# Optimization experiments

Measured on AMD Instinct MI355X. Metric: run time of the kernel, lower is better.

## Reference

```python
import jax, jax.numpy as jnp
import numpy as np

N = 50000
E = 800000
F_IN = 512
H = 128
K = 10
ALPHA = 0.1
EPS = 1e-5  # BatchNorm eps


def setup_inputs() -> dict:
    key = jax.random.key(0)
    ks = jax.random.split(key, 16)
    x = jax.random.normal(ks[0], (N, F_IN), dtype=jnp.float32)
    edge_index = jax.random.randint(ks[1], (2, E), 0, N, dtype=jnp.int64)
    # Linear weights (xavier-ish scale)
    W1 = jax.random.normal(ks[2], (F_IN, H), dtype=jnp.float32) * (1.0 / np.sqrt(F_IN))
    b1 = jnp.zeros((H,), dtype=jnp.float32)
    W2 = jax.random.normal(ks[3], (H, H), dtype=jnp.float32) * (1.0 / np.sqrt(H))
    b2 = jnp.zeros((H,), dtype=jnp.float32)
    # BatchNorm (eval mode: running stats)
    gamma1 = jnp.ones((H,), dtype=jnp.float32)
    beta1 = jnp.zeros((H,), dtype=jnp.float32)
    mean1 = jax.random.normal(ks[4], (H,), dtype=jnp.float32) * 0.1
    var1 = jax.random.uniform(ks[5], (H,), dtype=jnp.float32) + 0.5
    gamma2 = jnp.ones((H,), dtype=jnp.float32)
    beta2 = jnp.zeros((H,), dtype=jnp.float32)
    mean2 = jax.random.normal(ks[6], (H,), dtype=jnp.float32) * 0.1
    var2 = jax.random.uniform(ks[7], (H,), dtype=jnp.float32) + 0.5
    return {
        "x": x, "edge_index": edge_index,
        "W1": W1, "b1": b1, "gamma1": gamma1, "beta1": beta1, "mean1": mean1, "var1": var1,
        "W2": W2, "b2": b2, "gamma2": gamma2, "beta2": beta2, "mean2": mean2, "var2": var2,
    }


def _bn_eval(h, gamma, beta, mean, var):
    return (h - mean) * jax.lax.rsqrt(var + EPS) * gamma + beta


def _appnp_prop(h, edge_index):
    # add self loops
    loop = jnp.arange(N, dtype=edge_index.dtype)
    src = jnp.concatenate([edge_index[0], loop])
    dst = jnp.concatenate([edge_index[1], loop])
    # symmetric GCN normalization: deg^{-1/2}[src] * deg^{-1/2}[dst]
    deg = jax.ops.segment_sum(jnp.ones_like(src, dtype=h.dtype), dst, num_segments=N)
    dinv = jax.lax.rsqrt(jnp.maximum(deg, 1.0))
    norm = dinv[src] * dinv[dst]  # [E+N]
    h0 = h

    def step(carry, _):
        msg = carry[src] * norm[:, None]                    # [E+N, H]
        agg = jax.ops.segment_sum(msg, dst, num_segments=N)  # [N, H]
        return (1.0 - ALPHA) * agg + ALPHA * h0, None

    out, _ = jax.lax.scan(step, h, None, length=K)
    return out


def reference(x, edge_index, W1, b1, gamma1, beta1, mean1, var1,
              W2, b2, gamma2, beta2, mean2, var2):
    h = jax.nn.relu(x @ W1 + b1)
    h = _bn_eval(h, gamma1, beta1, mean1, var1)
    # dropout inactive (eval mode)
    h = h @ W2 + b2
    h = _bn_eval(h, gamma2, beta2, mean2, var2)
    return _appnp_prop(h, edge_index)
```

## Files before the change

kernel.cpp:

```cpp
#include <hip/hip_runtime.h>

#define ALPHA_F 0.1f
#define EPS_F   1e-5f

typedef float    f32x4 __attribute__((ext_vector_type(4)));
typedef _Float16 h16x8 __attribute__((ext_vector_type(8)));

__device__ __forceinline__ void gll16(const void* g, void* l)
{
    __builtin_amdgcn_global_load_lds(
        (const __attribute__((address_space(1))) void*)g,
        (__attribute__((address_space(3))) void*)l, 16, 0, 0);
}

__device__ __forceinline__ int pad_cnt(int d) { return (d + 8) & ~7; }

__global__ void convert_wstg(const float* __restrict__ W,
                             _Float16* __restrict__ Wstg, int K)
{
    int idx = blockIdx.x * 256 + threadIdx.x;
    if (idx < K * 128) {
        int k = idx >> 7, n = idx & 127;
        int i = k >> 5, kg = (k >> 3) & 3, j = k & 7;
        Wstg[(size_t)i * 4096 + (kg * 128 + n) * 8 + j] = (_Float16)W[idx];
    }
}

template<bool A_HALF, bool OUT_HALF>
__global__ __launch_bounds__(256) void gemm_stage_bn(
    const void* __restrict__ Av,
    const _Float16* __restrict__ Wstg,
    const float* __restrict__ bias,
    const float* __restrict__ gamma, const float* __restrict__ beta,
    const float* __restrict__ mean,  const float* __restrict__ var,
    void* __restrict__ outv, int M, int K, int do_relu)
{
    __shared__ __align__(16) char Abuf[2][8192];
    __shared__ __align__(16) char Wbuf[2][8192];

    const int t   = threadIdx.x;
    const int w   = t >> 6;
    const int l   = t & 63;
    const int l15 = l & 15;
    const int lk  = l >> 4;
    const int bm  = blockIdx.x * 64;
    const int nk  = K >> 5;
    const int row = w * 16 + l15;

    f32x4 acc[8];
#pragma unroll
    for (int f = 0; f < 8; ++f) acc[f] = (f32x4){0.f, 0.f, 0.f, 0.f};

    auto stage = [&](int buf, int i) {
        const char* wsrc = (const char*)Wstg + (size_t)i * 8192;
#pragma unroll
        for (int c = 0; c < 2; ++c) {
            const int base = w * 128 + c * 64;
            gll16(wsrc + (size_t)(base + l) * 16, &Wbuf[buf][base * 16]);
        }
        if (A_HALF) {
            const int base = w * 64;
            const int sl   = base + l;
            const int r    = sl >> 2;
            const int ch   = (sl & 3) ^ (r & 3);
            int gr = bm + r; gr = (gr < M) ? gr : (M - 1);
            const char* src = (const char*)Av + ((size_t)gr * K + i * 32) * 2
                              + (size_t)ch * 16;
            gll16(src, &Abuf[buf][base * 16]);
        } else {
#pragma unroll
            for (int c = 0; c < 2; ++c) {
                const int base = w * 128 + c * 64;
                const int sl   = base + l;
                const int r    = sl >> 3;
                const int ch   = (sl & 7) ^ (r & 7);
                int gr = bm + r; gr = (gr < M) ? gr : (M - 1);
                const char* src = (const char*)Av + ((size_t)gr * K + i * 32) * 4
                                  + (size_t)ch * 16;
                gll16(src, &Abuf[buf][base * 16]);
            }
        }
    };

    auto compute = [&](int buf) {
        h16x8 a;
        if (A_HALF) {
            a = *(const h16x8*)&Abuf[buf][(row * 4 + (lk ^ (row & 3))) * 16];
        } else {
            f32x4 a0 = *(const f32x4*)&Abuf[buf][(row * 8 + ((2 * lk)     ^ (row & 7))) * 16];
            f32x4 a1 = *(const f32x4*)&Abuf[buf][(row * 8 + ((2 * lk + 1) ^ (row & 7))) * 16];
#pragma unroll
            for (int j = 0; j < 4; ++j) {
                a[j]     = (_Float16)a0[j];
                a[4 + j] = (_Float16)a1[j];
            }
        }
#pragma unroll
        for (int f = 0; f < 8; ++f) {
            h16x8 b = *(const h16x8*)&Wbuf[buf][(lk * 128 + f * 16 + l15) * 16];
            acc[f] = __builtin_amdgcn_mfma_f32_16x16x32_f16(a, b, acc[f], 0, 0, 0);
        }
    };

    stage(0, 0);
    for (int i = 0; i < nk; ++i) {
        __syncthreads();
        if (i + 1 < nk) stage((i + 1) & 1, i + 1);
        compute(i & 1);
    }

#pragma unroll
    for (int f = 0; f < 8; ++f) {
        const int col = f * 16 + l15;
        float s  = gamma[col] * rsqrtf(var[col] + EPS_F);
        float sh = beta[col] - mean[col] * s;
        float bb = bias[col];
#pragma unroll
        for (int rr = 0; rr < 4; ++rr) {
            int rg = bm + w * 16 + lk * 4 + rr;
            if (rg < M) {
                float v = acc[f][rr] + bb;
                if (do_relu) v = fmaxf(v, 0.f);
                v = v * s + sh;
                if (OUT_HALF) ((_Float16*)outv)[(size_t)rg * 128 + col] = (_Float16)v;
                else          ((float*)outv)[(size_t)rg * 128 + col]    = v;
            }
        }
    }
}

__global__ void count_deg(const int* __restrict__ dst, int E, int* __restrict__ deg)
{
    int e = blockIdx.x * 256 + threadIdx.x;
    if (e < E) atomicAdd(&deg[dst[e]], 1);
}

__global__ __launch_bounds__(256) void scan_block_sums(
    const int* __restrict__ deg, int* __restrict__ bsum, int N)
{
    __shared__ int sh[256];
    const int t  = threadIdx.x;
    const int i0 = blockIdx.x * 1024 + t * 4;
    int s = 0;
    if (i0 + 3 < N) {
        int4 d4 = *(const int4*)(deg + i0);
        s = pad_cnt(d4.x) + pad_cnt(d4.y) + pad_cnt(d4.z) + pad_cnt(d4.w);
    } else {
#pragma unroll
        for (int j = 0; j < 4; ++j)
            if (i0 + j < N) s += pad_cnt(deg[i0 + j]);
    }
    sh[t] = s;
    __syncthreads();
#pragma unroll
    for (int d = 128; d > 0; d >>= 1) {
        if (t < d) sh[t] += sh[t + d];
        __syncthreads();
    }
    if (t == 0) bsum[blockIdx.x] = sh[0];
}

__global__ __launch_bounds__(256) void scan_offsets(
    const int* __restrict__ deg, const int* __restrict__ bsum,
    int* __restrict__ offs, int* __restrict__ cursor,
    float* __restrict__ dinv, int N, int B)
{
    __shared__ int sh[256];
    __shared__ int sbase;
    const int b = blockIdx.x, t = threadIdx.x;

    int v = (t < b && t < B) ? bsum[t] : 0;
    sh[t] = v;
    __syncthreads();
#pragma unroll
    for (int d = 128; d > 0; d >>= 1) {
        if (t < d) sh[t] += sh[t + d];
        __syncthreads();
    }
    if (t == 0) sbase = sh[0];
    __syncthreads();

    const int i0 = b * 1024 + t * 4;
    int c[4], s = 0;
#pragma unroll
    for (int j = 0; j < 4; ++j) {
        int i = i0 + j;
        c[j] = (i < N) ? pad_cnt(deg[i]) : 0;
        s += c[j];
    }
    sh[t] = s;
    __syncthreads();
    for (int d = 1; d < 256; d <<= 1) {
        int o = (t >= d) ? sh[t - d] : 0;
        __syncthreads();
        sh[t] += o;
        __syncthreads();
    }
    int run = sbase + sh[t] - s;
#pragma unroll
    for (int j = 0; j < 4; ++j) {
        int i = i0 + j;
        if (i < N) {
            offs[i]   = run;
            cursor[i] = run;
            dinv[i]   = rsqrtf((float)(deg[i] + 1));
            run += c[j];
        }
    }
    if (b == B - 1 && t == 255) offs[N] = run;
}

__global__ void scatter_csr(const int* __restrict__ src, const int* __restrict__ dst,
                            int E, const float* __restrict__ dinv,
                            int* __restrict__ cursor, int2* __restrict__ csr)
{
    int e = blockIdx.x * 256 + threadIdx.x;
    if (e < E) {
        int s = src[e], d = dst[e];
        int pos = atomicAdd(&cursor[d], 1);
        csr[pos] = make_int2(s, __float_as_int(dinv[s] * dinv[d]));
    }
}

__global__ void fill_self_pad(const int* __restrict__ offs, const int* __restrict__ deg,
                              const float* __restrict__ dinv,
                              int2* __restrict__ csr, int N)
{
    int i = blockIdx.x * 256 + threadIdx.x;
    if (i < N) {
        int base = offs[i], d = deg[i], end = offs[i + 1];
        float di = dinv[i];
        csr[base + d] = make_int2(i, __float_as_int(di * di));
        for (int p = base + d + 1; p < end; ++p)
            csr[p] = make_int2(i, 0);
    }
}

__global__ __launch_bounds__(256) void appnp_step(
    const _Float16* __restrict__ cur, const _Float16* __restrict__ h0,
    const int* __restrict__ offs, const int2* __restrict__ csr,
    _Float16* __restrict__ nxt, float* __restrict__ fout, int N)
{
    int wv = (int)((blockIdx.x * 256u + threadIdx.x) >> 6);
    if (wv >= N) return;
    const int i    = __builtin_amdgcn_readfirstlane(wv);
    const int lane = (int)(threadIdx.x & 63u);
    const int g    = lane >> 4;
    const int fl   = (lane & 15) * 8;

    int e   = offs[i];
    int end = offs[i + 1];

    f32x4 accL = (f32x4){0.f, 0.f, 0.f, 0.f};
    f32x4 accH = (f32x4){0.f, 0.f, 0.f, 0.f};

    int4 m = *(const int4*)(csr + e + 2 * g);
    int   iA = m.x,                     iB = m.z;
    float wA = __int_as_float(m.y),     wB = __int_as_float(m.w);
    h16x8 vA = *(const h16x8*)(cur + (size_t)iA * 128 + fl);
    h16x8 vB = *(const h16x8*)(cur + (size_t)iB * 128 + fl);

    for (e += 8; e < end; e += 8) {
        int4 m2 = *(const int4*)(csr + e + 2 * g);
        int   iA2 = m2.x,                 iB2 = m2.z;
        float wA2 = __int_as_float(m2.y), wB2 = __int_as_float(m2.w);
        h16x8 vA2 = *(const h16x8*)(cur + (size_t)iA2 * 128 + fl);
        h16x8 vB2 = *(const h16x8*)(cur + (size_t)iB2 * 128 + fl);
#pragma unroll
        for (int j = 0; j < 4; ++j) {
            accL[j] = fmaf(wA, (float)vA[j],     accL[j]);
            accH[j] = fmaf(wA, (float)vA[4 + j], accH[j]);
            accL[j] = fmaf(wB, (float)vB[j],     accL[j]);
            accH[j] = fmaf(wB, (float)vB[4 + j], accH[j]);
        }
        wA = wA2; wB = wB2; vA = vA2; vB = vB2;
    }
#pragma unroll
    for (int j = 0; j < 4; ++j) {
        accL[j] = fmaf(wA, (float)vA[j],     accL[j]);
        accH[j] = fmaf(wA, (float)vA[4 + j], accH[j]);
        accL[j] = fmaf(wB, (float)vB[j],     accL[j]);
        accH[j] = fmaf(wB, (float)vB[4 + j], accH[j]);
    }

#pragma unroll
    for (int j = 0; j < 4; ++j) {
        accL[j] += __shfl_xor(accL[j], 16);
        accL[j] += __shfl_xor(accL[j], 32);
        accH[j] += __shfl_xor(accH[j], 16);
        accH[j] += __shfl_xor(accH[j], 32);
    }

    if (lane < 16) {
        h16x8 hv = *(const h16x8*)(h0 + (size_t)i * 128 + fl);
        float o[8];
#pragma unroll
        for (int j = 0; j < 4; ++j) {
            o[j]     = ALPHA_F * (float)hv[j]     + (1.f - ALPHA_F) * accL[j];
            o[4 + j] = ALPHA_F * (float)hv[4 + j] + (1.f - ALPHA_F) * accH[j];
        }
        if (fout) {
            f32x4 o0, o1;
#pragma unroll
            for (int j = 0; j < 4; ++j) { o0[j] = o[j]; o1[j] = o[4 + j]; }
            *(f32x4*)(fout + (size_t)i * 128 + fl)     = o0;
            *(f32x4*)(fout + (size_t)i * 128 + fl + 4) = o1;
        } else {
            h16x8 o16;
#pragma unroll
            for (int j = 0; j < 8; ++j) o16[j] = (_Float16)o[j];
            *(h16x8*)(nxt + (size_t)i * 128 + fl) = o16;
        }
    }
}

static inline size_t align_up(size_t x) { return (x + 255) & ~(size_t)255; }

extern "C" void kernel_launch(void* const* d_in, const int* in_sizes, int n_in,
                              void* d_out, int out_size, void* d_ws, size_t ws_size,
                              hipStream_t stream)
{
    const float* x   = (const float*)d_in[0];
    const int*   ei  = (const int*)d_in[1];
    const float* W1  = (const float*)d_in[2];
    const float* b1  = (const float*)d_in[3];
    const float* g1  = (const float*)d_in[4];
    const float* be1 = (const float*)d_in[5];
    const float* m1  = (const float*)d_in[6];
    const float* v1  = (const float*)d_in[7];
    const float* W2  = (const float*)d_in[8];
    const float* b2  = (const float*)d_in[9];
    const float* g2  = (const float*)d_in[10];
    const float* be2 = (const float*)d_in[11];
    const float* m2  = (const float*)d_in[12];
    const float* v2  = (const float*)d_in[13];

    const int N = in_sizes[0] / 512;
    const int E = in_sizes[1] / 2;
    const int* src = ei;
    const int* dst = ei + E;
    const int CSR_CAP = E + 8 * N;
    const int NB = (N + 1023) / 1024;

    char* ws = (char*)d_ws;
    size_t off = 0;
    _Float16* hAh = (_Float16*)(ws + off); off += align_up((size_t)N * 128 * 2);
    _Float16* h0h = (_Float16*)(ws + off); off += align_up((size_t)N * 128 * 2);
    _Float16* p0  = (_Float16*)(ws + off); off += align_up((size_t)N * 128 * 2);
    _Float16* p1  = (_Float16*)(ws + off); off += align_up((size_t)N * 128 * 2);
    int*    deg  = (int*)(ws + off);    off += align_up((size_t)N * 4);
    float*  dinv = (float*)(ws + off);  off += align_up((size_t)N * 4);
    int*    offs = (int*)(ws + off);    off += align_up((size_t)(N + 1) * 4);
    int*    curs = (int*)(ws + off);    off += align_up((size_t)N * 4);
    int*    bsum = (int*)(ws + off);    off += align_up((size_t)256 * 4);
    int2*   csr  = (int2*)(ws + off);   off += align_up((size_t)CSR_CAP * 8);
    _Float16* w1s = (_Float16*)(ws + off); off += align_up((size_t)512 * 128 * 2);
    _Float16* w2s = (_Float16*)(ws + off); off += align_up((size_t)128 * 128 * 2);

    hipMemsetAsync(deg, 0, (size_t)N * 4, stream);
    count_deg<<<(E + 255) / 256, 256, 0, stream>>>(dst, E, deg);
    scan_block_sums<<<NB, 256, 0, stream>>>(deg, bsum, N);
    scan_offsets<<<NB, 256, 0, stream>>>(deg, bsum, offs, curs, dinv, N, NB);
    scatter_csr<<<(E + 255) / 256, 256, 0, stream>>>(src, dst, E, dinv, curs, csr);
    fill_self_pad<<<(N + 255) / 256, 256, 0, stream>>>(offs, deg, dinv, csr, N);

    convert_wstg<<<(512 * 128 + 255) / 256, 256, 0, stream>>>(W1, w1s, 512);
    convert_wstg<<<(128 * 128 + 255) / 256, 256, 0, stream>>>(W2, w2s, 128);

    gemm_stage_bn<false, true><<<(N + 63) / 64, 256, 0, stream>>>(
        x, w1s, b1, g1, be1, m1, v1, hAh, N, 512, 1);
    gemm_stage_bn<true, true><<<(N + 63) / 64, 256, 0, stream>>>(
        hAh, w2s, b2, g2, be2, m2, v2, h0h, N, 128, 0);

    const _Float16* cur = h0h;
    for (int k = 0; k < 10; ++k) {
        _Float16* nxt = (k & 1) ? p1 : p0;
        float* fo = (k == 9) ? (float*)d_out : nullptr;
        appnp_step<<<(N + 3) / 4, 256, 0, stream>>>(
            cur, h0h, offs, csr, nxt, fo, N);
        cur = nxt;
    }

    (void)n_in; (void)out_size; (void)ws_size;
}
```

Baseline: 438.2 us.

## Accumulate APPNP messages in packed fp16 and use persistent grid-stride waves

The propagation step now accumulates neighbor messages with packed half-precision FMAs instead of converting each value to fp32, halving the ALU work in the gather loop. It also launches a fixed grid of 8192 waves that loop over nodes instead of one wave per node, reducing block scheduling overhead. FP16 accumulation over many neighbors across ten iterations risks precision loss, and the fixed grid may reduce latency hiding for this memory-bound gather.

```diff
diff --git a/kernel.cpp b/kernel.cpp
--- a/kernel.cpp
+++ b/kernel.cpp
@@ -5,6 +5,7 @@
 
 typedef float    f32x4 __attribute__((ext_vector_type(4)));
 typedef _Float16 h16x8 __attribute__((ext_vector_type(8)));
+typedef _Float16 h16x2 __attribute__((ext_vector_type(2)));
 
 __device__ __forceinline__ void gll16(const void* g, void* l)
 {
@@ -236,80 +237,89 @@
     }
 }
 
+#define NWAVES 8192
+
 __global__ __launch_bounds__(256) void appnp_step(
     const _Float16* __restrict__ cur, const _Float16* __restrict__ h0,
     const int* __restrict__ offs, const int2* __restrict__ csr,
     _Float16* __restrict__ nxt, float* __restrict__ fout, int N)
 {
-    int wv = (int)((blockIdx.x * 256u + threadIdx.x) >> 6);
-    if (wv >= N) return;
-    const int i    = __builtin_amdgcn_readfirstlane(wv);
+    const int wv0  = __builtin_amdgcn_readfirstlane(
+                        (int)((blockIdx.x * 256u + threadIdx.x) >> 6));
     const int lane = (int)(threadIdx.x & 63u);
     const int g    = lane >> 4;
     const int fl   = (lane & 15) * 8;
 
-    int e   = offs[i];
-    int end = offs[i + 1];
-
-    f32x4 accL = (f32x4){0.f, 0.f, 0.f, 0.f};
-    f32x4 accH = (f32x4){0.f, 0.f, 0.f, 0.f};
-
-    int4 m = *(const int4*)(csr + e + 2 * g);
-    int   iA = m.x,                     iB = m.z;
-    float wA = __int_as_float(m.y),     wB = __int_as_float(m.w);
-    h16x8 vA = *(const h16x8*)(cur + (size_t)iA * 128 + fl);
-    h16x8 vB = *(const h16x8*)(cur + (size_t)iB * 128 + fl);
-
-    for (e += 8; e < end; e += 8) {
-        int4 m2 = *(const int4*)(csr + e + 2 * g);
-        int   iA2 = m2.x,                 iB2 = m2.z;
-        float wA2 = __int_as_float(m2.y), wB2 = __int_as_float(m2.w);
-        h16x8 vA2 = *(const h16x8*)(cur + (size_t)iA2 * 128 + fl);
-        h16x8 vB2 = *(const h16x8*)(cur + (size_t)iB2 * 128 + fl);
+    for (int i = wv0; i < N; i += NWAVES) {
+        int e   = offs[i];
+        int end = offs[i + 1];
+
+        h16x2 acc[4];
+#pragma unroll
+        for (int j = 0; j < 4; ++j) acc[j] = (h16x2){(_Float16)0, (_Float16)0};
+
+        int4 m = *(const int4*)(csr + e + 2 * g);
+        h16x8 vA = *(const h16x8*)(cur + (size_t)m.x * 128 + fl);
+        h16x8 vB = *(const h16x8*)(cur + (size_t)m.z * 128 + fl);
+
+        for (e += 8; e < end; e += 8) {
+            int4 m2 = *(const int4*)(csr + e + 2 * g);
+            h16x8 vA2 = *(const h16x8*)(cur + (size_t)m2.x * 128 + fl);
+            h16x8 vB2 = *(const h16x8*)(cur + (size_t)m2.z * 128 + fl);
+            _Float16 ha = (_Float16)__int_as_float(m.y);
+            _Float16 hb = (_Float16)__int_as_float(m.w);
+            h16x2 wa = (h16x2){ha, ha}, wb = (h16x2){hb, hb};
+#pragma unroll
+            for (int j = 0; j < 4; ++j) {
+                h16x2 va = (h16x2){vA[2 * j], vA[2 * j + 1]};
+                h16x2 vb = (h16x2){vB[2 * j], vB[2 * j + 1]};
+                acc[j] = __builtin_elementwise_fma(wa, va, acc[j]);
+                acc[j] = __builtin_elementwise_fma(wb, vb, acc[j]);
+            }
+            m = m2; vA = vA2; vB = vB2;
+        }
+        {
+            _Float16 ha = (_Float16)__int_as_float(m.y);
+            _Float16 hb = (_Float16)__int_as_float(m.w);
+            h16x2 wa = (h16x2){ha, ha}, wb = (h16x2){hb, hb};
+#pragma unroll
+            for (int j = 0; j < 4; ++j) {
+                h16x2 va = (h16x2){vA[2 * j], vA[2 * j + 1]};
+                h16x2 vb = (h16x2){vB[2 * j], vB[2 * j + 1]};
+                acc[j] = __builtin_elementwise_fma(wa, va, acc[j]);
+                acc[j] = __builtin_elementwise_fma(wb, vb, acc[j]);
+            }
+        }
+
+        float o[8];
 #pragma unroll
         for (int j = 0; j < 4; ++j) {
-            accL[j] = fmaf(wA, (float)vA[j],     accL[j]);
-            accH[j] = fmaf(wA, (float)vA[4 + j], accH[j]);
-            accL[j] = fmaf(wB, (float)vB[j],     accL[j]);
-            accH[j] = fmaf(wB, (float)vB[4 + j], accH[j]);
-        }
-        wA = wA2; wB = wB2; vA = vA2; vB = vB2;
-    }
-#pragma unroll
-    for (int j = 0; j < 4; ++j) {
-        accL[j] = fmaf(wA, (float)vA[j],     accL[j]);
-        accH[j] = fmaf(wA, (float)vA[4 + j], accH[j]);
-        accL[j] = fmaf(wB, (float)vB[j],     accL[j]);
-        accH[j] = fmaf(wB, (float)vB[4 + j], accH[j]);
-    }
-
-#pragma unroll
-    for (int j = 0; j < 4; ++j) {
-        accL[j] += __shfl_xor(accL[j], 16);
-        accL[j] += __shfl_xor(accL[j], 32);
-        accH[j] += __shfl_xor(accH[j], 16);
-        accH[j] += __shfl_xor(accH[j], 32);
-    }
-
-    if (lane < 16) {
-        h16x8 hv = *(const h16x8*)(h0 + (size_t)i * 128 + fl);
-        float o[8];
-#pragma unroll
-        for (int j = 0; j < 4; ++j) {
-            o[j]     = ALPHA_F * (float)hv[j]     + (1.f - ALPHA_F) * accL[j];
-            o[4 + j] = ALPHA_F * (float)hv[4 + j] + (1.f - ALPHA_F) * accH[j];
-        }
-        if (fout) {
-            f32x4 o0, o1;
-#pragma unroll
-            for (int j = 0; j < 4; ++j) { o0[j] = o[j]; o1[j] = o[4 + j]; }
-            *(f32x4*)(fout + (size_t)i * 128 + fl)     = o0;
-            *(f32x4*)(fout + (size_t)i * 128 + fl + 4) = o1;
-        } else {
-            h16x8 o16;
-#pragma unroll
-            for (int j = 0; j < 8; ++j) o16[j] = (_Float16)o[j];
-            *(h16x8*)(nxt + (size_t)i * 128 + fl) = o16;
+            o[2 * j]     = (float)acc[j][0];
+            o[2 * j + 1] = (float)acc[j][1];
+        }
+#pragma unroll
+        for (int j = 0; j < 8; ++j) {
+            o[j] += __shfl_xor(o[j], 16);
+            o[j] += __shfl_xor(o[j], 32);
+        }
+
+        if (lane < 16) {
+            h16x8 hv = *(const h16x8*)(h0 + (size_t)i * 128 + fl);
+#pragma unroll
+            for (int j = 0; j < 8; ++j)
+                o[j] = ALPHA_F * (float)hv[j] + (1.f - ALPHA_F) * o[j];
+            if (fout) {
+                f32x4 o0, o1;
+#pragma unroll
+                for (int j = 0; j < 4; ++j) { o0[j] = o[j]; o1[j] = o[4 + j]; }
+                *(f32x4*)(fout + (size_t)i * 128 + fl)     = o0;
+                *(f32x4*)(fout + (size_t)i * 128 + fl + 4) = o1;
+            } else {
+                h16x8 o16;
+#pragma unroll
+                for (int j = 0; j < 8; ++j) o16[j] = (_Float16)o[j];
+                *(h16x8*)(nxt + (size_t)i * 128 + fl) = o16;
+            }
         }
     }
 }
@@ -376,7 +386,7 @@
     for (int k = 0; k < 10; ++k) {
         _Float16* nxt = (k & 1) ? p1 : p0;
         float* fo = (k == 9) ? (float*)d_out : nullptr;
-        appnp_step<<<(N + 3) / 4, 256, 0, stream>>>(
+        appnp_step<<<NWAVES / 4, 256, 0, stream>>>(
             cur, h0h, offs, csr, nxt, fo, N);
         cur = nxt;
     }
```

New measurement: 430.0 us. Within noise of the previous version (-1.9%).

## Slice features into 4 column blocks and pack CSR entries into 32 bits

Applied to the files above, without the earlier changes.

The propagation state is re-laid out into four 32-feature slices, each stored contiguously per node, so that each block works on one slice and that slice's gather working set is a quarter the size and more likely to stay in cache. CSR entries are packed into 4 bytes: a 16-bit source index plus an fp16 edge weight. This halves edge-list traffic but assumes N fits in 16 bits and lowers weight precision. The step kernel now uses a persistent grid-stride loop with 8 edges per wave iteration and 4 features per lane. An extra reslice kernel is added before the loop.

```diff
diff --git a/kernel.cpp b/kernel.cpp
--- a/kernel.cpp
+++ b/kernel.cpp
@@ -5,6 +5,7 @@
 
 typedef float    f32x4 __attribute__((ext_vector_type(4)));
 typedef _Float16 h16x8 __attribute__((ext_vector_type(8)));
+typedef _Float16 h16x4 __attribute__((ext_vector_type(4)));
 
 __device__ __forceinline__ void gll16(const void* g, void* l)
 {
@@ -14,6 +15,13 @@
 }
 
 __device__ __forceinline__ int pad_cnt(int d) { return (d + 8) & ~7; }
+
+__device__ __forceinline__ unsigned pack_csr(int s, float w)
+{
+    _Float16 h = (_Float16)w;
+    return (unsigned)(s & 0xFFFF)
+         | ((unsigned)__builtin_bit_cast(unsigned short, h) << 16);
+}
 
 __global__ void convert_wstg(const float* __restrict__ W,
                              _Float16* __restrict__ Wstg, int K)
@@ -129,6 +137,19 @@
     }
 }
 
+__global__ void reslice(const _Float16* __restrict__ src,
+                        _Float16* __restrict__ dst, int N)
+{
+    int idx = blockIdx.x * 256 + threadIdx.x;
+    if (idx < N * 16) {
+        int i = idx >> 4;
+        int f = (idx & 15) * 8;
+        int s = f >> 5, wi = f & 31;
+        h16x8 v = *(const h16x8*)(src + (size_t)i * 128 + f);
+        *(h16x8*)(dst + ((size_t)s * N + i) * 32 + wi) = v;
+    }
+}
+
 __global__ void count_deg(const int* __restrict__ dst, int E, int* __restrict__ deg)
 {
     int e = blockIdx.x * 256 + threadIdx.x;
@@ -212,104 +233,95 @@
 
 __global__ void scatter_csr(const int* __restrict__ src, const int* __restrict__ dst,
                             int E, const float* __restrict__ dinv,
-                            int* __restrict__ cursor, int2* __restrict__ csr)
+                            int* __restrict__ cursor, unsigned* __restrict__ csr4)
 {
     int e = blockIdx.x * 256 + threadIdx.x;
     if (e < E) {
         int s = src[e], d = dst[e];
         int pos = atomicAdd(&cursor[d], 1);
-        csr[pos] = make_int2(s, __float_as_int(dinv[s] * dinv[d]));
+        csr4[pos] = pack_csr(s, dinv[s] * dinv[d]);
     }
 }
 
 __global__ void fill_self_pad(const int* __restrict__ offs, const int* __restrict__ deg,
                               const float* __restrict__ dinv,
-                              int2* __restrict__ csr, int N)
+                              unsigned* __restrict__ csr4, int N)
 {
     int i = blockIdx.x * 256 + threadIdx.x;
     if (i < N) {
         int base = offs[i], d = deg[i], end = offs[i + 1];
         float di = dinv[i];
-        csr[base + d] = make_int2(i, __float_as_int(di * di));
+        csr4[base + d] = pack_csr(i, di * di);
         for (int p = base + d + 1; p < end; ++p)
-            csr[p] = make_int2(i, 0);
-    }
-}
-
-__global__ __launch_bounds__(256) void appnp_step(
-    const _Float16* __restrict__ cur, const _Float16* __restrict__ h0,
-    const int* __restrict__ offs, const int2* __restrict__ csr,
+            csr4[p] = pack_csr(i, 0.f);
+    }
+}
+
+#define WAVES_PER_SLICE 2048
+
+__global__ __launch_bounds__(256) void appnp_step_s(
+    const _Float16* __restrict__ cur,
+    const _Float16* __restrict__ h0q,
+    const int* __restrict__ offs, const unsigned* __restrict__ csr4,
     _Float16* __restrict__ nxt, float* __restrict__ fout, int N)
 {
-    int wv = (int)((blockIdx.x * 256u + threadIdx.x) >> 6);
-    if (wv >= N) return;
-    const int i    = __builtin_amdgcn_readfirstlane(wv);
+    const int s    = blockIdx.x & 3;
+    const int wis  = (blockIdx.x >> 2) * 4 + (threadIdx.x >> 6);
     const int lane = (int)(threadIdx.x & 63u);
-    const int g    = lane >> 4;
-    const int fl   = (lane & 15) * 8;
-
-    int e   = offs[i];
-    int end = offs[i + 1];
-
-    f32x4 accL = (f32x4){0.f, 0.f, 0.f, 0.f};
-    f32x4 accH = (f32x4){0.f, 0.f, 0.f, 0.f};
-
-    int4 m = *(const int4*)(csr + e + 2 * g);
-    int   iA = m.x,                     iB = m.z;
-    float wA = __int_as_float(m.y),     wB = __int_as_float(m.w);
-    h16x8 vA = *(const h16x8*)(cur + (size_t)iA * 128 + fl);
-    h16x8 vB = *(const h16x8*)(cur + (size_t)iB * 128 + fl);
-
-    for (e += 8; e < end; e += 8) {
-        int4 m2 = *(const int4*)(csr + e + 2 * g);
-        int   iA2 = m2.x,                 iB2 = m2.z;
-        float wA2 = __int_as_float(m2.y), wB2 = __int_as_float(m2.w);
-        h16x8 vA2 = *(const h16x8*)(cur + (size_t)iA2 * 128 + fl);
-        h16x8 vB2 = *(const h16x8*)(cur + (size_t)iB2 * 128 + fl);
+    const int q    = lane & 7;
+    const int eo   = lane >> 3;
+
+    const _Float16* curs = cur + (size_t)s * N * 32;
+    const _Float16* h0s  = h0q + (size_t)s * N * 32;
+    _Float16*       nxts = nxt + (size_t)s * N * 32;
+
+    for (int i = wis; i < N; i += WAVES_PER_SLICE) {
+        int e   = offs[i];
+        int end = offs[i + 1];
+
+        float acc[4] = {0.f, 0.f, 0.f, 0.f};
+
+        unsigned m = csr4[e + eo];
+        h16x4 v = *(const h16x4*)(curs + (size_t)(m & 0xFFFFu) * 32 + q * 4);
+
+        for (e += 8; e < end; e += 8) {
+            unsigned m2 = csr4[e + eo];
+            h16x4 v2 = *(const h16x4*)(curs + (size_t)(m2 & 0xFFFFu) * 32 + q * 4);
+            float w = (float)__builtin_bit_cast(_Float16, (unsigned short)(m >> 16));
+#pragma unroll
+            for (int j = 0; j < 4; ++j) acc[j] = fmaf(w, (float)v[j], acc[j]);
+            m = m2; v = v2;
+        }
+        {
+            float w = (float)__builtin_bit_cast(_Float16, (unsigned short)(m >> 16));
+#pragma unroll
+            for (int j = 0; j < 4; ++j) acc[j] = fmaf(w, (float)v[j], acc[j]);
+        }
+
 #pragma unroll
         for (int j = 0; j < 4; ++j) {
-            accL[j] = fmaf(wA, (float)vA[j],     accL[j]);
-            accH[j] = fmaf(wA, (float)vA[4 + j], accH[j]);
-            accL[j] = fmaf(wB, (float)vB[j],     accL[j]);
-            accH[j] = fmaf(wB, (float)vB[4 + j], accH[j]);
-        }
-        wA = wA2; wB = wB2; vA = vA2; vB = vB2;
-    }
-#pragma unroll
-    for (int j = 0; j < 4; ++j) {
-        accL[j] = fmaf(wA, (float)vA[j],     accL[j]);
-        accH[j] = fmaf(wA, (float)vA[4 + j], accH[j]);
-        accL[j] = fmaf(wB, (float)vB[j],     accL[j]);
-        accH[j] = fmaf(wB, (float)vB[4 + j], accH[j]);
-    }
-
-#pragma unroll
-    for (int j = 0; j < 4; ++j) {
-        accL[j] += __shfl_xor(accL[j], 16);
-        accL[j] += __shfl_xor(accL[j], 32);
-        accH[j] += __shfl_xor(accH[j], 16);
-        accH[j] += __shfl_xor(accH[j], 32);
-    }
-
-    if (lane < 16) {
-        h16x8 hv = *(const h16x8*)(h0 + (size_t)i * 128 + fl);
-        float o[8];
-#pragma unroll
-        for (int j = 0; j < 4; ++j) {
-            o[j]     = ALPHA_F * (float)hv[j]     + (1.f - ALPHA_F) * accL[j];
-            o[4 + j] = ALPHA_F * (float)hv[4 + j] + (1.f - ALPHA_F) * accH[j];
-        }
-        if (fout) {
-            f32x4 o0, o1;
-#pragma unroll
-            for (int j = 0; j < 4; ++j) { o0[j] = o[j]; o1[j] = o[4 + j]; }
-            *(f32x4*)(fout + (size_t)i * 128 + fl)     = o0;
-            *(f32x4*)(fout + (size_t)i * 128 + fl + 4) = o1;
-        } else {
-            h16x8 o16;
-#pragma unroll
-            for (int j = 0; j < 8; ++j) o16[j] = (_Float16)o[j];
-            *(h16x8*)(nxt + (size_t)i * 128 + fl) = o16;
+            acc[j] += __shfl_xor(acc[j], 8);
+            acc[j] += __shfl_xor(acc[j], 16);
+            acc[j] += __shfl_xor(acc[j], 32);
+        }
+
+        if (lane < 8) {
+            h16x4 hv = *(const h16x4*)(h0s + (size_t)i * 32 + q * 4);
+            float o[4];
+#pragma unroll
+            for (int j = 0; j < 4; ++j)
+                o[j] = ALPHA_F * (float)hv[j] + (1.f - ALPHA_F) * acc[j];
+            if (fout) {
+                f32x4 o4;
+#pragma unroll
+                for (int j = 0; j < 4; ++j) o4[j] = o[j];
+                *(f32x4*)(fout + (size_t)i * 128 + s * 32 + q * 4) = o4;
+            } else {
+                h16x4 o16;
+#pragma unroll
+                for (int j = 0; j < 4; ++j) o16[j] = (_Float16)o[j];
+                *(h16x4*)(nxts + (size_t)i * 32 + q * 4) = o16;
+            }
         }
     }
 }
@@ -346,14 +358,15 @@
     size_t off = 0;
     _Float16* hAh = (_Float16*)(ws + off); off += align_up((size_t)N * 128 * 2);
     _Float16* h0h = (_Float16*)(ws + off); off += align_up((size_t)N * 128 * 2);
-    _Float16* p0  = (_Float16*)(ws + off); off += align_up((size_t)N * 128 * 2);
-    _Float16* p1  = (_Float16*)(ws + off); off += align_up((size_t)N * 128 * 2);
+    _Float16* h0q = (_Float16*)(ws + off); off += align_up((size_t)N * 128 * 2);
+    _Float16* q1  = (_Float16*)(ws + off); off += align_up((size_t)N * 128 * 2);
+    _Float16* q2  = (_Float16*)(ws + off); off += align_up((size_t)N * 128 * 2);
     int*    deg  = (int*)(ws + off);    off += align_up((size_t)N * 4);
     float*  dinv = (float*)(ws + off);  off += align_up((size_t)N * 4);
     int*    offs = (int*)(ws + off);    off += align_up((size_t)(N + 1) * 4);
     int*    curs = (int*)(ws + off);    off += align_up((size_t)N * 4);
     int*    bsum = (int*)(ws + off);    off += align_up((size_t)256 * 4);
-    int2*   csr  = (int2*)(ws + off);   off += align_up((size_t)CSR_CAP * 8);
+    unsigned* csr4 = (unsigned*)(ws + off); off += align_up((size_t)CSR_CAP * 4);
     _Float16* w1s = (_Float16*)(ws + off); off += align_up((size_t)512 * 128 * 2);
     _Float16* w2s = (_Float16*)(ws + off); off += align_up((size_t)128 * 128 * 2);
 
@@ -361,8 +374,8 @@
     count_deg<<<(E + 255) / 256, 256, 0, stream>>>(dst, E, deg);
     scan_block_sums<<<NB, 256, 0, stream>>>(deg, bsum, N);
     scan_offsets<<<NB, 256, 0, stream>>>(deg, bsum, offs, curs, dinv, N, NB);
-    scatter_csr<<<(E + 255) / 256, 256, 0, stream>>>(src, dst, E, dinv, curs, csr);
-    fill_self_pad<<<(N + 255) / 256, 256, 0, stream>>>(offs, deg, dinv, csr, N);
+    scatter_csr<<<(E + 255) / 256, 256, 0, stream>>>(src, dst, E, dinv, curs, csr4);
+    fill_self_pad<<<(N + 255) / 256, 256, 0, stream>>>(offs, deg, dinv, csr4, N);
 
     convert_wstg<<<(512 * 128 + 255) / 256, 256, 0, stream>>>(W1, w1s, 512);
     convert_wstg<<<(128 * 128 + 255) / 256, 256, 0, stream>>>(W2, w2s, 128);
@@ -372,12 +385,14 @@
     gemm_stage_bn<true, true><<<(N + 63) / 64, 256, 0, stream>>>(
         hAh, w2s, b2, g2, be2, m2, v2, h0h, N, 128, 0);
 
-    const _Float16* cur = h0h;
+    reslice<<<(N * 16 + 255) / 256, 256, 0, stream>>>(h0h, h0q, N);
+
+    const _Float16* cur = h0q;
     for (int k = 0; k < 10; ++k) {
-        _Float16* nxt = (k & 1) ? p1 : p0;
+        _Float16* nxt = (k & 1) ? q2 : q1;
         float* fo = (k == 9) ? (float*)d_out : nullptr;
-        appnp_step<<<(N + 3) / 4, 256, 0, stream>>>(
-            cur, h0h, offs, csr, nxt, fo, N);
+        appnp_step_s<<<WAVES_PER_SLICE * 4 / 4, 256, 0, stream>>>(
+            cur, h0q, offs, csr4, nxt, fo, N);
         cur = nxt;
     }
 
```

Measured after the change: 660.8 us. 1.51x slower.
